# Optimization experiments

Measured on AMD Instinct MI355X. Metric: run time of the kernel, lower is better.

Reference implementation:

```python
import jax, jax.numpy as jnp
import numpy as np

N_NODES = 50000
N_EDGES = 800000
D_IN = 128
D_OUT = 128
N_MLP = 2


def _lin(x, W, b):
    return x @ W.T + b


def setup_inputs() -> dict:
    key = jax.random.key(0)
    ks = jax.random.split(key, 32)
    d = {}
    d['feat'] = jax.random.normal(ks[0], (N_NODES, D_IN), dtype=jnp.float32)
    d['src'] = jax.random.randint(ks[1], (N_EDGES,), 0, N_NODES, dtype=jnp.int32)
    d['dst'] = jax.random.randint(ks[2], (N_EDGES,), 0, N_NODES, dtype=jnp.int32)
    s_in = 1.0 / np.sqrt(D_IN)
    s_out = 1.0 / np.sqrt(D_OUT)
    i = 3
    def w(shape, s):
        nonlocal i
        out = jax.random.normal(ks[i], shape, dtype=jnp.float32) * s
        i += 1
        return out
    for nm in ['asrc', 'adst', 'asub', 'amul']:
        d['W_' + nm] = w((D_OUT, D_IN), s_in)
        d['b_' + nm] = w((D_OUT,), s_in)
    d['W_aout'] = w((1, D_OUT), s_out)
    d['b_aout'] = w((1,), s_out)
    for nm in ['pool', 'pool2']:
        d['W_' + nm] = w((D_IN, D_IN), s_in)
        d['b_' + nm] = w((D_IN,), s_in)
    for nm in ['self', 'neigh', 'neigh2']:
        d['W_' + nm] = w((D_OUT, D_IN), s_in)
        d['b_' + nm] = w((D_OUT,), s_in)
    d['W_mlp'] = w((N_MLP, D_OUT, D_OUT), s_out)
    d['b_mlp'] = w((N_MLP, D_OUT), s_out)
    return d


def reference(feat, src, dst,
              W_asrc, b_asrc, W_adst, b_adst, W_asub, b_asub, W_amul, b_amul,
              W_aout, b_aout, W_pool, b_pool, W_pool2, b_pool2,
              W_self, b_self, W_neigh, b_neigh, W_neigh2, b_neigh2,
              W_mlp, b_mlp):
    gelu = lambda x: jax.nn.gelu(x, approximate=False)
    fs = feat[src]            # [E, D_IN] gathered source feats
    fd = feat[dst]            # [E, D_IN] gathered dest feats
    # edge attention score
    e = _lin(fs - fd, W_asub, b_asub) + _lin(fs * fd, W_amul, b_amul)
    e = e + _lin(feat, W_asrc, b_asrc)[src] + _lin(feat, W_adst, b_adst)[dst]
    e = gelu(e)
    e = jax.nn.leaky_relu(_lin(e, W_aout, b_aout), 0.2)  # [E, 1]
    deg = jax.ops.segment_sum(jnp.ones((src.shape[0],), jnp.float32), dst,
                              num_segments=N_NODES)      # in-degree
    has_in = (deg > 0)[:, None]
    # max-pool branch
    h = gelu(_lin(feat, W_pool, b_pool))
    m = e * h[src]
    neigh = jax.ops.segment_max(m, dst, num_segments=N_NODES)
    neigh = jnp.where(has_in, neigh, 0.0)
    # mean-pool branch
    h2 = gelu(_lin(feat, W_pool2, b_pool2))
    m2 = e * h2[src]
    neigh2 = jax.ops.segment_sum(m2, dst, num_segments=N_NODES)
    neigh2 = neigh2 / jnp.maximum(deg, 1.0)[:, None]
    rst = _lin(feat, W_self, b_self) + _lin(neigh, W_neigh, b_neigh) \
        + _lin(neigh2, W_neigh2, b_neigh2)
    for li in range(W_mlp.shape[0]):
        rst = rst + _lin(gelu(rst), W_mlp[li], b_mlp[li])
    return rst
```

## Files before the change

kernel.cpp:

```cpp
#include <hip/hip_runtime.h>
#include <cstdint>
#include <cstddef>

#define NN 50000
#define NE 800000
#define DD 128

#define NBK 391
#define BSLOT 4096

static_assert(NN % 16 == 0, "node tiles");
static_assert(NE % 16 == 0, "edge tiles");
static_assert(((NN + 127) >> 7) == NBK, "bucket count");

typedef __bf16 bf16_t;
typedef bf16_t bf16x8 __attribute__((ext_vector_type(8)));
typedef bf16_t bf16x4 __attribute__((ext_vector_type(4)));
typedef float f32x4 __attribute__((ext_vector_type(4)));
typedef float f32x16 __attribute__((ext_vector_type(16)));

__device__ __forceinline__ float gelu_f(float x) {
    float u = x * x;
    float t = fmaf(u, -0.1029442445f, -2.3021184019f);
    float s = __builtin_amdgcn_exp2f(x * t);
    return x * __builtin_amdgcn_rcpf(1.0f + s);
}

__device__ __forceinline__ int frag_idx(int ch, int k) {
    int t = ch >> 4, n = ch & 15;
    int kb = k >> 5, r = k & 31, q = r >> 3, j = r & 7;
    return ((((t * 4 + kb) * 4 + q) * 16 + n) << 3) + j;
}

__device__ __forceinline__ int frag32_idx(int ch, int k) {
    int t = ch >> 5, m = ch & 31;
    int kc = k >> 4, q = (k >> 3) & 1, j = k & 7;
    return ((((t * 8 + kc) * 2 + q) * 32 + m) << 3) + j;
}

__global__ __launch_bounds__(256) void convert_feat_kernel(
    const float* __restrict__ feat, bf16_t* __restrict__ fb)
{
    int i = blockIdx.x * 256 + threadIdx.x;
    f32x4 v = ((const f32x4*)feat)[i];
    bf16x4 o;
    o[0] = (bf16_t)v[0]; o[1] = (bf16_t)v[1]; o[2] = (bf16_t)v[2]; o[3] = (bf16_t)v[3];
    ((bf16x4*)fb)[i] = o;
}

__global__ __launch_bounds__(256) void prep_kernel(
    const float* __restrict__ W_asrc, const float* __restrict__ b_asrc,
    const float* __restrict__ W_adst, const float* __restrict__ b_adst,
    const float* __restrict__ W_asub, const float* __restrict__ b_asub,
    const float* __restrict__ W_amul, const float* __restrict__ b_amul,
    const float* __restrict__ W_pool, const float* __restrict__ W_pool2,
    const float* __restrict__ W_self, const float* __restrict__ b_self,
    const float* __restrict__ W_neigh, const float* __restrict__ b_neigh,
    const float* __restrict__ W_neigh2, const float* __restrict__ b_neigh2,
    const float* __restrict__ W_mlp,
    bf16_t* __restrict__ W_Sf, bf16_t* __restrict__ W_Df, bf16_t* __restrict__ W_amulf,
    bf16_t* __restrict__ W_poolf, bf16_t* __restrict__ W_pool2f,
    bf16_t* __restrict__ W_selff, bf16_t* __restrict__ W_neighf, bf16_t* __restrict__ W_neigh2f,
    bf16_t* __restrict__ W_mlpf,
    float* __restrict__ b_e, float* __restrict__ b_rst)
{
    int gid = blockIdx.x * 256 + threadIdx.x;
    float sub = W_asub[gid];
    int ch = gid >> 7, k = gid & 127;
    int fi = frag_idx(ch, k);
    W_Sf[fi] = (bf16_t)(W_asrc[gid] + sub);
    W_Df[fi] = (bf16_t)(W_adst[gid] - sub);
    W_amulf[frag32_idx(ch, k)] = (bf16_t)W_amul[gid];
    W_poolf[fi]   = (bf16_t)W_pool[gid];
    W_pool2f[fi]  = (bf16_t)W_pool2[gid];
    W_selff[fi]   = (bf16_t)W_self[gid];
    W_neighf[fi]  = (bf16_t)W_neigh[gid];
    W_neigh2f[fi] = (bf16_t)W_neigh2[gid];
    W_mlpf[fi]            = (bf16_t)W_mlp[gid];
    W_mlpf[DD * DD + fi]  = (bf16_t)W_mlp[DD * DD + gid];
    if (gid < DD) {
        b_e[gid]   = b_asub[gid] + b_amul[gid] + b_asrc[gid] + b_adst[gid];
        b_rst[gid] = b_self[gid] + b_neigh[gid] + b_neigh2[gid];
    }
}

__global__ __launch_bounds__(256) void scatter_bucket_kernel(
    const int* __restrict__ src, const int* __restrict__ dst,
    int* __restrict__ gcursor, int2* __restrict__ ebuf)
{
    __shared__ int cnt[NBK];
    __shared__ int ofs[NBK];
    int t = threadIdx.x;
    for (int b = t; b < NBK; b += 256) cnt[b] = 0;
    __syncthreads();
    int qbase = blockIdx.x * 1024 + t;
    int4 s4[4], d4[4];
    bool valid[4];
#pragma unroll
    for (int k = 0; k < 4; k++) {
        int q = qbase + k * 256;
        valid[k] = q < NE / 4;
        if (valid[k]) {
            s4[k] = ((const int4*)src)[q];
            d4[k] = ((const int4*)dst)[q];
#pragma unroll
            for (int j = 0; j < 4; j++)
                atomicAdd(&cnt[((&d4[k].x)[j]) >> 7], 1);
        }
    }
    __syncthreads();
    for (int b = t; b < NBK; b += 256) {
        int c = cnt[b];
        ofs[b] = c ? atomicAdd(&gcursor[b], c) : 0;
    }
    __syncthreads();
#pragma unroll
    for (int k = 0; k < 4; k++) {
        if (valid[k]) {
#pragma unroll
            for (int j = 0; j < 4; j++) {
                int d = (&d4[k].x)[j];
                int b = d >> 7;
                int p = atomicAdd(&ofs[b], 1);
                int2 pk;
                pk.x = (&s4[k].x)[j];
                pk.y = d;
                ebuf[(size_t)b * BSLOT + p] = pk;
            }
        }
    }
}

__global__ __launch_bounds__(512) void bucket_scan_kernel(
    const int* __restrict__ gcursor, int* __restrict__ boff)
{
    __shared__ int tmp[512];
    int t = threadIdx.x;
    int v = (t < NBK) ? gcursor[t] : 0;
    tmp[t] = v;
    __syncthreads();
#pragma unroll
    for (int d = 1; d < 512; d <<= 1) {
        int x = (t >= d) ? tmp[t - d] : 0;
        __syncthreads();
        tmp[t] += x;
        __syncthreads();
    }
    if (t < NBK) boff[t] = tmp[t] - v;
}

__global__ __launch_bounds__(256) void finalize_csr_kernel(
    const int2* __restrict__ ebuf, const int* __restrict__ gcursor, const int* __restrict__ boff,
    int2* __restrict__ csr, int* __restrict__ offsets, int* __restrict__ deg)
{
    __shared__ int lcnt[128];
    __shared__ int nbase[128];
    __shared__ int pre[128];
    int B = blockIdx.x, t = threadIdx.x;
    int v0 = B << 7;
    int cnt = gcursor[B];
    int dbase = boff[B];
    const int2* eb = ebuf + (size_t)B * BSLOT;
    if (t < 128) lcnt[t] = 0;
    __syncthreads();
    for (int i = t; i < cnt; i += 256)
        atomicAdd(&lcnt[eb[i].y - v0], 1);
    __syncthreads();
    int c = (t < 128) ? lcnt[t] : 0;
    if (t < 128) pre[t] = c;
    __syncthreads();
#pragma unroll
    for (int d = 1; d < 128; d <<= 1) {
        int x = (t >= d && t < 128) ? pre[t - d] : 0;
        __syncthreads();
        if (t < 128) pre[t] += x;
        __syncthreads();
    }
    if (t < 128) {
        int nb = dbase + pre[t] - c;
        nbase[t] = nb;
        int v = v0 + t;
        if (v < NN) { offsets[v] = nb; deg[v] = c; }
        lcnt[t] = 0;
    }
    __syncthreads();
    for (int i = t; i < cnt; i += 256) {
        int2 pk = eb[i];
        int j = pk.y - v0;
        int pos = nbase[j] + atomicAdd(&lcnt[j], 1);
        csr[pos] = pk;
    }
}

__device__ __forceinline__ void mm16_store_ilv(
    const bf16x8 a[4], const bf16_t* __restrict__ Wf, const float* __restrict__ bias,
    bf16_t* __restrict__ hh, int nb, int n, int q, int lane, int sub)
{
#pragma unroll
    for (int t = 0; t < 8; t++) {
        f32x4 acc = {0.f, 0.f, 0.f, 0.f};
#pragma unroll
        for (int kb = 0; kb < 4; kb++) {
            bf16x8 b = *(const bf16x8*)(Wf + (((t * 4 + kb) * 64 + lane) << 3));
            acc = __builtin_amdgcn_mfma_f32_16x16x32_bf16(a[kb], b, acc, 0, 0, 0);
        }
        int ch = t * 16 + n;
        int pos = ((ch >> 1) << 2) + (ch & 1) + sub;
        float bv = bias[ch];
#pragma unroll
        for (int r = 0; r < 4; r++)
            hh[(size_t)(nb + q * 4 + r) * 256 + pos] = (bf16_t)gelu_f(acc[r] + bv);
    }
}

__device__ __forceinline__ void mm16_store_plain(
    const bf16x8 a[4], const bf16_t* __restrict__ Wf, const float* __restrict__ bias,
    bf16_t* __restrict__ out, int nb, int n, int q, int lane)
{
#pragma unroll
    for (int t = 0; t < 8; t++) {
        f32x4 acc = {0.f, 0.f, 0.f, 0.f};
#pragma unroll
        for (int kb = 0; kb < 4; kb++) {
            bf16x8 b = *(const bf16x8*)(Wf + (((t * 4 + kb) * 64 + lane) << 3));
            acc = __builtin_amdgcn_mfma_f32_16x16x32_bf16(a[kb], b, acc, 0, 0, 0);
        }
        int ch = t * 16 + n;
        float bv = bias ? bias[ch] : 0.0f;
#pragma unroll
        for (int r = 0; r < 4; r++)
            out[(size_t)(nb + q * 4 + r) * DD + ch] = (bf16_t)(acc[r] + bv);
    }
}

__global__ __launch_bounds__(256) void node_linear_kernel(
    const bf16_t* __restrict__ fb,
    const bf16_t* __restrict__ W_poolf, const float* __restrict__ b_pool,
    const bf16_t* __restrict__ W_pool2f, const float* __restrict__ b_pool2,
    const bf16_t* __restrict__ W_Sf, const float* __restrict__ b_e,
    const bf16_t* __restrict__ W_Df,
    bf16_t* __restrict__ hh, bf16_t* __restrict__ us, bf16_t* __restrict__ ud)
{
    int wid = blockIdx.x * 4 + (threadIdx.x >> 6);
    if (wid >= NN / 16) return;
    int lane = threadIdx.x & 63, n = lane & 15, q = lane >> 4;
    int nb = wid * 16;
    bf16x8 a[4];
#pragma unroll
    for (int kb = 0; kb < 4; kb++)
        a[kb] = *(const bf16x8*)(fb + (size_t)(nb + n) * DD + kb * 32 + q * 8);
    mm16_store_ilv(a, W_poolf, b_pool, hh, nb, n, q, lane, 0);
    mm16_store_ilv(a, W_pool2f, b_pool2, hh, nb, n, q, lane, 2);
    mm16_store_plain(a, W_Sf, b_e, us, nb, n, q, lane);
    mm16_store_plain(a, W_Df, nullptr, ud, nb, n, q, lane);
}

#define ES_NBLK 2500
#define ES_ITERS (NE / 32 / ES_NBLK)

__global__ __launch_bounds__(256, 4) void edge_score_kernel(
    const bf16_t* __restrict__ fb,
    const bf16_t* __restrict__ us, const bf16_t* __restrict__ ud,
    const bf16_t* __restrict__ W_amulf,
    const float* __restrict__ w_aout, const float* __restrict__ b_aout,
    int2* __restrict__ csr)
{
    __shared__ __align__(16) bf16_t sP[2][32 * 128];
    __shared__ __align__(16) bf16_t sU[2][32 * 128];
    __shared__ float partials[32 * 5];
    __shared__ float sWa[128];
    int tid = threadIdx.x;
    int wave = tid >> 6, lane = tid & 63;
    int n = lane & 31, q = lane >> 5;
    int t = wave;

    if (tid < 128) sWa[tid] = w_aout[tid];

    bf16x8 wAm[8];
#pragma unroll
    for (int kc = 0; kc < 8; kc++)
        wAm[kc] = *(const bf16x8*)(W_amulf + ((((t * 8 + kc) * 2 + q) * 32 + n) << 3));
    float bout = b_aout[0];

    int sed0 = tid >> 4, sc = tid & 15;

    int e0 = blockIdx.x * 32;
    int2 pk0 = csr[e0 + sed0];
    int2 pk1 = csr[e0 + sed0 + 16];
    bf16x8 pfs0 = *(const bf16x8*)(fb + (size_t)pk0.x * DD + sc * 8);
    bf16x8 pfd0 = *(const bf16x8*)(fb + (size_t)pk0.y * DD + sc * 8);
    bf16x8 pus0 = *(const bf16x8*)(us + (size_t)pk0.x * DD + sc * 8);
    bf16x8 pud0 = *(const bf16x8*)(ud + (size_t)pk0.y * DD + sc * 8);
    bf16x8 pfs1 = *(const bf16x8*)(fb + (size_t)pk1.x * DD + sc * 8);
    bf16x8 pfd1 = *(const bf16x8*)(fb + (size_t)pk1.y * DD + sc * 8);
    bf16x8 pus1 = *(const bf16x8*)(us + (size_t)pk1.x * DD + sc * 8);
    bf16x8 pud1 = *(const bf16x8*)(ud + (size_t)pk1.y * DD + sc * 8);

    for (int it = 0; it < ES_ITERS; it++) {
        int buf = it & 1;
        int eb = (blockIdx.x + it * ES_NBLK) * 32;
        {
            bf16x8 pp, uu;
#pragma unroll
            for (int j = 0; j < 8; j++) {
                pp[j] = (bf16_t)((float)pfs0[j] * (float)pfd0[j]);
                uu[j] = (bf16_t)((float)pus0[j] + (float)pud0[j]);
            }
            int ph = (sc ^ (sed0 & 7)) << 3;
            *(bf16x8*)(sP[buf] + sed0 * 128 + ph) = pp;
            *(bf16x8*)(sU[buf] + sed0 * 128 + ph) = uu;
        }
        {
            int ed = sed0 + 16;
            bf16x8 pp, uu;
#pragma unroll
            for (int j = 0; j < 8; j++) {
                pp[j] = (bf16_t)((float)pfs1[j] * (float)pfd1[j]);
                uu[j] = (bf16_t)((float)pus1[j] + (float)pud1[j]);
            }
            int ph = (sc ^ (ed & 7)) << 3;
            *(bf16x8*)(sP[buf] + ed * 128 + ph) = pp;
            *(bf16x8*)(sU[buf] + ed * 128 + ph) = uu;
        }
        __syncthreads();
        if (it + 1 < ES_ITERS) {
            int e1 = (blockIdx.x + (it + 1) * ES_NBLK) * 32;
            pk0 = csr[e1 + sed0];
            pk1 = csr[e1 + sed0 + 16];
            pfs0 = *(const bf16x8*)(fb + (size_t)pk0.x * DD + sc * 8);
            pfd0 = *(const bf16x8*)(fb + (size_t)pk0.y * DD + sc * 8);
            pus0 = *(const bf16x8*)(us + (size_t)pk0.x * DD + sc * 8);
            pud0 = *(const bf16x8*)(ud + (size_t)pk0.y * DD + sc * 8);
            pfs1 = *(const bf16x8*)(fb + (size_t)pk1.x * DD + sc * 8);
            pfd1 = *(const bf16x8*)(fb + (size_t)pk1.y * DD + sc * 8);
            pus1 = *(const bf16x8*)(us + (size_t)pk1.x * DD + sc * 8);
            pud1 = *(const bf16x8*)(ud + (size_t)pk1.y * DD + sc * 8);
        }
        f32x16 acc = {};
        int swz = n & 7;
#pragma unroll
        for (int kc = 0; kc < 8; kc++) {
            bf16x8 bP = *(const bf16x8*)(sP[buf] + n * 128 + (((kc * 2 + q) ^ swz) << 3));
            acc = __builtin_amdgcn_mfma_f32_32x32x16_bf16(wAm[kc], bP, acc, 0, 0, 0);
        }
        float psum = 0.f;
#pragma unroll
        for (int c = 0; c < 4; c++) {
            bf16x4 sv = *(const bf16x4*)(sU[buf] + n * 128 + (((t * 4 + c) ^ swz) << 3) + q * 4);
            f32x4 wv = *(const f32x4*)(sWa + t * 32 + c * 8 + q * 4);
#pragma unroll
            for (int j = 0; j < 4; j++)
                psum = fmaf(gelu_f(acc[c * 4 + j] + (float)sv[j]), wv[j], psum);
        }
        psum += __shfl_xor(psum, 32, 64);
        if (lane < 32) partials[lane * 5 + wave] = psum;
        __syncthreads();
        if (wave == (it & 3) && lane < 32) {
            const float* pr = partials + lane * 5;
            float s = pr[0] + pr[1] + pr[2] + pr[3] + bout;
            s = s > 0.f ? s : 0.2f * s;
            csr[eb + lane].y = __float_as_int(s);
        }
    }
}

__global__ __launch_bounds__(256) void aggregate_kernel(
    const bf16_t* __restrict__ hh,
    const int* __restrict__ offsets, const int* __restrict__ deg,
    const int2* __restrict__ csr,
    bf16_t* __restrict__ neigh, bf16_t* __restrict__ neigh2)
{
    int wave = threadIdx.x >> 6, lane = threadIdx.x & 63;
    int v = blockIdx.x * 4 + wave;
    if (v >= NN) return;
    int off = offsets[v];
    int dg = deg[v];
    int quarter = lane >> 4;
    int cl = lane & 15;
    float mx[8], sm[8];
#pragma unroll
    for (int j = 0; j < 8; j++) { mx[j] = -INFINITY; sm[j] = 0.f; }
    for (int base = 0; base < dg; base += 64) {
        int cnt = dg - base; if (cnt > 64) cnt = 64;
        int s_l = 0; float sc_l = 0.f;
        if (lane < cnt) {
            int2 pk = csr[off + base + lane];
            s_l = pk.x;
            sc_l = __int_as_float(pk.y);
        }
        int nit = (cnt + 3) >> 2;
#pragma unroll 2
        for (int i = 0; i < nit; i++) {
            int idx = 4 * i + quarter;
            int s = __shfl(s_l, idx, 64);
            float sc = __shfl(sc_l, idx, 64);
            if (idx < cnt) {
                const bf16_t* row = hh + (size_t)s * 256 + 16 * cl;
                bf16x8 h0 = *(const bf16x8*)(row);
                bf16x8 h1 = *(const bf16x8*)(row + 8);
                mx[0] = fmaxf(mx[0], sc * (float)h0[0]);
                mx[1] = fmaxf(mx[1], sc * (float)h0[1]);
                sm[0] = fmaf(sc, (float)h0[2], sm[0]);
                sm[1] = fmaf(sc, (float)h0[3], sm[1]);
                mx[2] = fmaxf(mx[2], sc * (float)h0[4]);
                mx[3] = fmaxf(mx[3], sc * (float)h0[5]);
                sm[2] = fmaf(sc, (float)h0[6], sm[2]);
                sm[3] = fmaf(sc, (float)h0[7], sm[3]);
                mx[4] = fmaxf(mx[4], sc * (float)h1[0]);
                mx[5] = fmaxf(mx[5], sc * (float)h1[1]);
                sm[4] = fmaf(sc, (float)h1[2], sm[4]);
                sm[5] = fmaf(sc, (float)h1[3], sm[5]);
                mx[6] = fmaxf(mx[6], sc * (float)h1[4]);
                mx[7] = fmaxf(mx[7], sc * (float)h1[5]);
                sm[6] = fmaf(sc, (float)h1[6], sm[6]);
                sm[7] = fmaf(sc, (float)h1[7], sm[7]);
            }
        }
    }
#pragma unroll
    for (int j = 0; j < 8; j++) {
        mx[j] = fmaxf(mx[j], __shfl_xor(mx[j], 16, 64));
        mx[j] = fmaxf(mx[j], __shfl_xor(mx[j], 32, 64));
        sm[j] += __shfl_xor(sm[j], 16, 64);
        sm[j] += __shfl_xor(sm[j], 32, 64);
    }
    if (quarter == 0) {
        float inv = 1.0f / (float)(dg > 1 ? dg : 1);
        bf16x8 n1, n2;
#pragma unroll
        for (int j = 0; j < 8; j++) {
            n1[j] = (bf16_t)(dg > 0 ? mx[j] : 0.0f);
            n2[j] = (bf16_t)(sm[j] * inv);
        }
        *(bf16x8*)(neigh + (size_t)v * DD + 8 * cl) = n1;
        *(bf16x8*)(neigh2 + (size_t)v * DD + 8 * cl) = n2;
    }
}

__global__ __launch_bounds__(256) void final_kernel(
    const bf16_t* __restrict__ fb, const bf16_t* __restrict__ neigh, const bf16_t* __restrict__ neigh2,
    const bf16_t* __restrict__ W_selff, const bf16_t* __restrict__ W_neighf, const bf16_t* __restrict__ W_neigh2f,
    const float* __restrict__ b_rst,
    const bf16_t* __restrict__ W_mlpf, const float* __restrict__ b_mlp,
    float* __restrict__ out)
{
    __shared__ __align__(16) float lds[4][16 * 132];
    int wave = threadIdx.x >> 6;
    int wid = blockIdx.x * 4 + wave;
    if (wid >= NN / 16) return;
    int lane = threadIdx.x & 63, n = lane & 15, q = lane >> 4;
    int nb = wid * 16;
    float* L = lds[wave];

    bf16x8 af[4], an[4], am[4];
#pragma unroll
    for (int kb = 0; kb < 4; kb++) {
        size_t o = (size_t)(nb + n) * DD + kb * 32 + q * 8;
        af[kb] = *(const bf16x8*)(fb + o);
        an[kb] = *(const bf16x8*)(neigh + o);
        am[kb] = *(const bf16x8*)(neigh2 + o);
    }
    f32x4 rst[8];
#pragma unroll
    for (int t = 0; t < 8; t++) {
        f32x4 acc = {0.f, 0.f, 0.f, 0.f};
#pragma unroll
        for (int kb = 0; kb < 4; kb++) {
            int wo = ((t * 4 + kb) * 64 + lane) << 3;
            acc = __builtin_amdgcn_mfma_f32_16x16x32_bf16(af[kb], *(const bf16x8*)(W_selff + wo), acc, 0, 0, 0);
            acc = __builtin_amdgcn_mfma_f32_16x16x32_bf16(an[kb], *(const bf16x8*)(W_neighf + wo), acc, 0, 0, 0);
            acc = __builtin_amdgcn_mfma_f32_16x16x32_bf16(am[kb], *(const bf16x8*)(W_neigh2f + wo), acc, 0, 0, 0);
        }
        float bv = b_rst[t * 16 + n];
#pragma unroll
        for (int r = 0; r < 4; r++) acc[r] += bv;
        rst[t] = acc;
    }

#pragma unroll
    for (int li = 0; li < 2; li++) {
#pragma unroll
        for (int t = 0; t < 8; t++)
#pragma unroll
            for (int r = 0; r < 4; r++)
                L[(q * 4 + r) * 132 + t * 16 + n] = gelu_f(rst[t][r]);
        __builtin_amdgcn_wave_barrier();
        bf16x8 g[4];
#pragma unroll
        for (int kb = 0; kb < 4; kb++) {
            const f32x4* p = (const f32x4*)&L[n * 132 + kb * 32 + q * 8];
            f32x4 x0 = p[0], x1 = p[1];
            bf16x8 gg;
            gg[0] = (bf16_t)x0[0]; gg[1] = (bf16_t)x0[1]; gg[2] = (bf16_t)x0[2]; gg[3] = (bf16_t)x0[3];
            gg[4] = (bf16_t)x1[0]; gg[5] = (bf16_t)x1[1]; gg[6] = (bf16_t)x1[2]; gg[7] = (bf16_t)x1[3];
            g[kb] = gg;
        }
        __builtin_amdgcn_wave_barrier();
        const bf16_t* Wl = W_mlpf + li * DD * DD;
#pragma unroll
        for (int t = 0; t < 8; t++) {
            f32x4 acc = {0.f, 0.f, 0.f, 0.f};
#pragma unroll
            for (int kb = 0; kb < 4; kb++) {
                bf16x8 b = *(const bf16x8*)(Wl + (((t * 4 + kb) * 64 + lane) << 3));
                acc = __builtin_amdgcn_mfma_f32_16x16x32_bf16(g[kb], b, acc, 0, 0, 0);
            }
            float bm = b_mlp[li * DD + t * 16 + n];
#pragma unroll
            for (int r = 0; r < 4; r++) rst[t][r] += acc[r] + bm;
        }
    }

#pragma unroll
    for (int t = 0; t < 8; t++)
#pragma unroll
        for (int r = 0; r < 4; r++)
            out[(size_t)(nb + q * 4 + r) * DD + t * 16 + n] = rst[t][r];
}

extern "C" void kernel_launch(void* const* d_in, const int* in_sizes, int n_in,
                              void* d_out, int out_size, void* d_ws, size_t ws_size,
                              hipStream_t stream)
{
    const float* feat    = (const float*)d_in[0];
    const int*   src     = (const int*)d_in[1];
    const int*   dst     = (const int*)d_in[2];
    const float* W_asrc  = (const float*)d_in[3],  *b_asrc  = (const float*)d_in[4];
    const float* W_adst  = (const float*)d_in[5],  *b_adst  = (const float*)d_in[6];
    const float* W_asub  = (const float*)d_in[7],  *b_asub  = (const float*)d_in[8];
    const float* W_amul  = (const float*)d_in[9],  *b_amul  = (const float*)d_in[10];
    const float* W_aout  = (const float*)d_in[11], *b_aout  = (const float*)d_in[12];
    const float* W_pool  = (const float*)d_in[13], *b_pool  = (const float*)d_in[14];
    const float* W_pool2 = (const float*)d_in[15], *b_pool2 = (const float*)d_in[16];
    const float* W_self  = (const float*)d_in[17], *b_self  = (const float*)d_in[18];
    const float* W_neigh = (const float*)d_in[19], *b_neigh = (const float*)d_in[20];
    const float* W_neigh2= (const float*)d_in[21], *b_neigh2= (const float*)d_in[22];
    const float* W_mlp   = (const float*)d_in[23], *b_mlp   = (const float*)d_in[24];
    float* out = (float*)d_out;

    char* w = (char*)d_ws;
    auto take = [&](size_t bytes) -> void* {
        void* p = (void*)w;
        w += (bytes + 255) & ~(size_t)255;
        return p;
    };
    bf16_t* fb      = (bf16_t*)take((size_t)NN * DD * sizeof(bf16_t));
    bf16_t* neigh   = (bf16_t*)take((size_t)NN * DD * sizeof(bf16_t));
    bf16_t* neigh2  = (bf16_t*)take((size_t)NN * DD * sizeof(bf16_t));
    bf16_t* hh      = (bf16_t*)take((size_t)NN * 256 * sizeof(bf16_t));
    bf16_t* us      = (bf16_t*)take((size_t)NN * DD * sizeof(bf16_t));
    bf16_t* ud      = (bf16_t*)take((size_t)NN * DD * sizeof(bf16_t));
    int*    deg     = (int*)take((size_t)NN * sizeof(int));
    int*    offsets = (int*)take((size_t)NN * sizeof(int));
    int2*   csr     = (int2*)take((size_t)NE * sizeof(int2));
    int2*   ebuf    = (int2*)take((size_t)NBK * BSLOT * sizeof(int2));
    int*    gcursor = (int*)take((size_t)NBK * sizeof(int));
    int*    boff    = (int*)take((size_t)NBK * sizeof(int));
    bf16_t* W_Sf    = (bf16_t*)take((size_t)DD * DD * sizeof(bf16_t));
    bf16_t* W_Df    = (bf16_t*)take((size_t)DD * DD * sizeof(bf16_t));
    bf16_t* W_amulf = (bf16_t*)take((size_t)DD * DD * sizeof(bf16_t));
    bf16_t* W_poolf = (bf16_t*)take((size_t)DD * DD * sizeof(bf16_t));
    bf16_t* W_pool2f= (bf16_t*)take((size_t)DD * DD * sizeof(bf16_t));
    bf16_t* W_selff = (bf16_t*)take((size_t)DD * DD * sizeof(bf16_t));
    bf16_t* W_neighf= (bf16_t*)take((size_t)DD * DD * sizeof(bf16_t));
    bf16_t* W_neigh2f=(bf16_t*)take((size_t)DD * DD * sizeof(bf16_t));
    bf16_t* W_mlpf  = (bf16_t*)take((size_t)2 * DD * DD * sizeof(bf16_t));
    float*  b_e     = (float*)take((size_t)DD * sizeof(float));
    float*  b_rst   = (float*)take((size_t)DD * sizeof(float));

    (void)hipMemsetAsync(gcursor, 0, (size_t)NBK * sizeof(int), stream);

    convert_feat_kernel<<<NN * DD / 4 / 256, 256, 0, stream>>>(feat, fb);

    prep_kernel<<<DD * DD / 256, 256, 0, stream>>>(
        W_asrc, b_asrc, W_adst, b_adst, W_asub, b_asub, W_amul, b_amul,
        W_pool, W_pool2, W_self, b_self, W_neigh, b_neigh, W_neigh2, b_neigh2, W_mlp,
        W_Sf, W_Df, W_amulf, W_poolf, W_pool2f, W_selff, W_neighf, W_neigh2f, W_mlpf,
        b_e, b_rst);

    scatter_bucket_kernel<<<(NE / 4 + 1023) / 1024, 256, 0, stream>>>(src, dst, gcursor, ebuf);
    bucket_scan_kernel<<<1, 512, 0, stream>>>(gcursor, boff);
    finalize_csr_kernel<<<NBK, 256, 0, stream>>>(ebuf, gcursor, boff, csr, offsets, deg);

    const int nwaves = NN / 16;
    const int ngrid = (nwaves + 3) / 4;
    node_linear_kernel<<<ngrid, 256, 0, stream>>>(
        fb, W_poolf, b_pool, W_pool2f, b_pool2, W_Sf, b_e, W_Df, hh, us, ud);

    edge_score_kernel<<<ES_NBLK, 256, 0, stream>>>(
        fb, us, ud, W_amulf, W_aout, b_aout, csr);

    aggregate_kernel<<<(NN + 3) / 4, 256, 0, stream>>>(
        hh, offsets, deg, csr, neigh, neigh2);

    final_kernel<<<ngrid, 256, 0, stream>>>(
        fb, neigh, neigh2, W_selff, W_neighf, W_neigh2f, b_rst, W_mlpf, b_mlp, out);
}
```

Baseline: 359.2 us.

## Compute source-side attention projection per edge instead of precomputing node table

Stops precomputing the per-node source projection table 'us' in the node linear kernel. The edge score kernel now applies W_Sf directly to the gathered source features with a second MFMA per k-chunk, and adds the bias inside the kernel. This drops one node-sized store and one random per-edge gather of 256 bytes, at the cost of doubling edge-level MFMA work, extra LDS staging and more registers for the weight fragments (occupancy hint lowered from 4 to 3).

```diff
diff --git a/kernel.cpp b/kernel.cpp
--- a/kernel.cpp
+++ b/kernel.cpp
@@ -68,9 +68,10 @@
     float sub = W_asub[gid];
     int ch = gid >> 7, k = gid & 127;
     int fi = frag_idx(ch, k);
-    W_Sf[fi] = (bf16_t)(W_asrc[gid] + sub);
+    int fi32 = frag32_idx(ch, k);
+    W_Sf[fi32] = (bf16_t)(W_asrc[gid] + sub);
     W_Df[fi] = (bf16_t)(W_adst[gid] - sub);
-    W_amulf[frag32_idx(ch, k)] = (bf16_t)W_amul[gid];
+    W_amulf[fi32] = (bf16_t)W_amul[gid];
     W_poolf[fi]   = (bf16_t)W_pool[gid];
     W_pool2f[fi]  = (bf16_t)W_pool2[gid];
     W_selff[fi]   = (bf16_t)W_self[gid];
@@ -237,9 +238,8 @@
     const bf16_t* __restrict__ fb,
     const bf16_t* __restrict__ W_poolf, const float* __restrict__ b_pool,
     const bf16_t* __restrict__ W_pool2f, const float* __restrict__ b_pool2,
-    const bf16_t* __restrict__ W_Sf, const float* __restrict__ b_e,
     const bf16_t* __restrict__ W_Df,
-    bf16_t* __restrict__ hh, bf16_t* __restrict__ us, bf16_t* __restrict__ ud)
+    bf16_t* __restrict__ hh, bf16_t* __restrict__ ud)
 {
     int wid = blockIdx.x * 4 + (threadIdx.x >> 6);
     if (wid >= NN / 16) return;
@@ -251,35 +251,39 @@
         a[kb] = *(const bf16x8*)(fb + (size_t)(nb + n) * DD + kb * 32 + q * 8);
     mm16_store_ilv(a, W_poolf, b_pool, hh, nb, n, q, lane, 0);
     mm16_store_ilv(a, W_pool2f, b_pool2, hh, nb, n, q, lane, 2);
-    mm16_store_plain(a, W_Sf, b_e, us, nb, n, q, lane);
     mm16_store_plain(a, W_Df, nullptr, ud, nb, n, q, lane);
 }
 
 #define ES_NBLK 2500
 #define ES_ITERS (NE / 32 / ES_NBLK)
 
-__global__ __launch_bounds__(256, 4) void edge_score_kernel(
-    const bf16_t* __restrict__ fb,
-    const bf16_t* __restrict__ us, const bf16_t* __restrict__ ud,
-    const bf16_t* __restrict__ W_amulf,
+__global__ __launch_bounds__(256, 3) void edge_score_kernel(
+    const bf16_t* __restrict__ fb, const bf16_t* __restrict__ ud,
+    const bf16_t* __restrict__ W_amulf, const bf16_t* __restrict__ W_Sf,
     const float* __restrict__ w_aout, const float* __restrict__ b_aout,
+    const float* __restrict__ b_e,
     int2* __restrict__ csr)
 {
     __shared__ __align__(16) bf16_t sP[2][32 * 128];
-    __shared__ __align__(16) bf16_t sU[2][32 * 128];
+    __shared__ __align__(16) bf16_t sS[2][32 * 128];
+    __shared__ __align__(16) bf16_t sUd[2][32 * 128];
     __shared__ float partials[32 * 5];
     __shared__ float sWa[128];
+    __shared__ float sBe[128];
     int tid = threadIdx.x;
     int wave = tid >> 6, lane = tid & 63;
     int n = lane & 31, q = lane >> 5;
     int t = wave;
 
-    if (tid < 128) sWa[tid] = w_aout[tid];
-
-    bf16x8 wAm[8];
-#pragma unroll
-    for (int kc = 0; kc < 8; kc++)
-        wAm[kc] = *(const bf16x8*)(W_amulf + ((((t * 8 + kc) * 2 + q) * 32 + n) << 3));
+    if (tid < 128) { sWa[tid] = w_aout[tid]; sBe[tid] = b_e[tid]; }
+
+    bf16x8 wAm[8], wSf[8];
+#pragma unroll
+    for (int kc = 0; kc < 8; kc++) {
+        int wo = (((t * 8 + kc) * 2 + q) * 32 + n) << 3;
+        wAm[kc] = *(const bf16x8*)(W_amulf + wo);
+        wSf[kc] = *(const bf16x8*)(W_Sf + wo);
+    }
     float bout = b_aout[0];
 
     int sed0 = tid >> 4, sc = tid & 15;
@@ -289,38 +293,34 @@
     int2 pk1 = csr[e0 + sed0 + 16];
     bf16x8 pfs0 = *(const bf16x8*)(fb + (size_t)pk0.x * DD + sc * 8);
     bf16x8 pfd0 = *(const bf16x8*)(fb + (size_t)pk0.y * DD + sc * 8);
-    bf16x8 pus0 = *(const bf16x8*)(us + (size_t)pk0.x * DD + sc * 8);
     bf16x8 pud0 = *(const bf16x8*)(ud + (size_t)pk0.y * DD + sc * 8);
     bf16x8 pfs1 = *(const bf16x8*)(fb + (size_t)pk1.x * DD + sc * 8);
     bf16x8 pfd1 = *(const bf16x8*)(fb + (size_t)pk1.y * DD + sc * 8);
-    bf16x8 pus1 = *(const bf16x8*)(us + (size_t)pk1.x * DD + sc * 8);
     bf16x8 pud1 = *(const bf16x8*)(ud + (size_t)pk1.y * DD + sc * 8);
 
     for (int it = 0; it < ES_ITERS; it++) {
         int buf = it & 1;
         int eb = (blockIdx.x + it * ES_NBLK) * 32;
         {
-            bf16x8 pp, uu;
-#pragma unroll
-            for (int j = 0; j < 8; j++) {
+            bf16x8 pp;
+#pragma unroll
+            for (int j = 0; j < 8; j++)
                 pp[j] = (bf16_t)((float)pfs0[j] * (float)pfd0[j]);
-                uu[j] = (bf16_t)((float)pus0[j] + (float)pud0[j]);
-            }
             int ph = (sc ^ (sed0 & 7)) << 3;
             *(bf16x8*)(sP[buf] + sed0 * 128 + ph) = pp;
-            *(bf16x8*)(sU[buf] + sed0 * 128 + ph) = uu;
+            *(bf16x8*)(sS[buf] + sed0 * 128 + ph) = pfs0;
+            *(bf16x8*)(sUd[buf] + sed0 * 128 + ph) = pud0;
         }
         {
             int ed = sed0 + 16;
-            bf16x8 pp, uu;
-#pragma unroll
-            for (int j = 0; j < 8; j++) {
+            bf16x8 pp;
+#pragma unroll
+            for (int j = 0; j < 8; j++)
                 pp[j] = (bf16_t)((float)pfs1[j] * (float)pfd1[j]);
-                uu[j] = (bf16_t)((float)pus1[j] + (float)pud1[j]);
-            }
             int ph = (sc ^ (ed & 7)) << 3;
             *(bf16x8*)(sP[buf] + ed * 128 + ph) = pp;
-            *(bf16x8*)(sU[buf] + ed * 128 + ph) = uu;
+            *(bf16x8*)(sS[buf] + ed * 128 + ph) = pfs1;
+            *(bf16x8*)(sUd[buf] + ed * 128 + ph) = pud1;
         }
         __syncthreads();
         if (it + 1 < ES_ITERS) {
@@ -329,28 +329,28 @@
             pk1 = csr[e1 + sed0 + 16];
             pfs0 = *(const bf16x8*)(fb + (size_t)pk0.x * DD + sc * 8);
             pfd0 = *(const bf16x8*)(fb + (size_t)pk0.y * DD + sc * 8);
-            pus0 = *(const bf16x8*)(us + (size_t)pk0.x * DD + sc * 8);
             pud0 = *(const bf16x8*)(ud + (size_t)pk0.y * DD + sc * 8);
             pfs1 = *(const bf16x8*)(fb + (size_t)pk1.x * DD + sc * 8);
             pfd1 = *(const bf16x8*)(fb + (size_t)pk1.y * DD + sc * 8);
-            pus1 = *(const bf16x8*)(us + (size_t)pk1.x * DD + sc * 8);
             pud1 = *(const bf16x8*)(ud + (size_t)pk1.y * DD + sc * 8);
         }
         f32x16 acc = {};
         int swz = n & 7;
 #pragma unroll
         for (int kc = 0; kc < 8; kc++) {
-            bf16x8 bP = *(const bf16x8*)(sP[buf] + n * 128 + (((kc * 2 + q) ^ swz) << 3));
-            acc = __builtin_amdgcn_mfma_f32_32x32x16_bf16(wAm[kc], bP, acc, 0, 0, 0);
+            int off = n * 128 + (((kc * 2 + q) ^ swz) << 3);
+            acc = __builtin_amdgcn_mfma_f32_32x32x16_bf16(wAm[kc], *(const bf16x8*)(sP[buf] + off), acc, 0, 0, 0);
+            acc = __builtin_amdgcn_mfma_f32_32x32x16_bf16(wSf[kc], *(const bf16x8*)(sS[buf] + off), acc, 0, 0, 0);
         }
         float psum = 0.f;
 #pragma unroll
         for (int c = 0; c < 4; c++) {
-            bf16x4 sv = *(const bf16x4*)(sU[buf] + n * 128 + (((t * 4 + c) ^ swz) << 3) + q * 4);
+            bf16x4 sv = *(const bf16x4*)(sUd[buf] + n * 128 + (((t * 4 + c) ^ swz) << 3) + q * 4);
             f32x4 wv = *(const f32x4*)(sWa + t * 32 + c * 8 + q * 4);
+            f32x4 bv = *(const f32x4*)(sBe + t * 32 + c * 8 + q * 4);
 #pragma unroll
             for (int j = 0; j < 4; j++)
-                psum = fmaf(gelu_f(acc[c * 4 + j] + (float)sv[j]), wv[j], psum);
+                psum = fmaf(gelu_f(acc[c * 4 + j] + (float)sv[j] + bv[j]), wv[j], psum);
         }
         psum += __shfl_xor(psum, 32, 64);
         if (lane < 32) partials[lane * 5 + wave] = psum;
@@ -548,7 +548,6 @@
     bf16_t* neigh   = (bf16_t*)take((size_t)NN * DD * sizeof(bf16_t));
     bf16_t* neigh2  = (bf16_t*)take((size_t)NN * DD * sizeof(bf16_t));
     bf16_t* hh      = (bf16_t*)take((size_t)NN * 256 * sizeof(bf16_t));
-    bf16_t* us      = (bf16_t*)take((size_t)NN * DD * sizeof(bf16_t));
     bf16_t* ud      = (bf16_t*)take((size_t)NN * DD * sizeof(bf16_t));
     int*    deg     = (int*)take((size_t)NN * sizeof(int));
     int*    offsets = (int*)take((size_t)NN * sizeof(int));
@@ -585,10 +584,10 @@
     const int nwaves = NN / 16;
     const int ngrid = (nwaves + 3) / 4;
     node_linear_kernel<<<ngrid, 256, 0, stream>>>(
-        fb, W_poolf, b_pool, W_pool2f, b_pool2, W_Sf, b_e, W_Df, hh, us, ud);
+        fb, W_poolf, b_pool, W_pool2f, b_pool2, W_Df, hh, ud);
 
     edge_score_kernel<<<ES_NBLK, 256, 0, stream>>>(
-        fb, us, ud, W_amulf, W_aout, b_aout, csr);
+        fb, ud, W_amulf, W_Sf, W_aout, b_aout, b_e, csr);
 
     aggregate_kernel<<<(NN + 3) / 4, 256, 0, stream>>>(
         hh, offsets, deg, csr, neigh, neigh2);
```

Measured after the change: 366.1 us. Within noise of the previous version (+1.9%).
